# Kernel tuning notes

Hardware: AMD Instinct MI355X
Metric: run time of the kernel (lower is better)

Reference implementation:

```python
import jax, jax.numpy as jnp
import numpy as np

PRED_STEPS = 12
N_NEG = 100
TEMP = 0.1
EPS = 1e-12


def _l2norm(x):
    # matches torch F.normalize(dim=-1): x / max(||x||, eps)
    n = jnp.sqrt(jnp.sum(x * x, axis=-1, keepdims=True))
    return x / jnp.maximum(n, EPS)


def setup_inputs() -> dict:
    key = jax.random.key(0)
    k1, k2, k3, k4 = jax.random.split(key, 4)
    B, T, D = 8, 256, 256
    context = jax.random.normal(k1, (B, T, D), dtype=jnp.float32)
    targets = jax.random.normal(k2, (B, T, D), dtype=jnp.float32)
    W = jax.random.normal(k3, (PRED_STEPS, D, D), dtype=jnp.float32) * (1.0 / np.sqrt(D))
    b = jax.random.normal(k4, (PRED_STEPS, D), dtype=jnp.float32) * 0.01
    return {"context": context, "targets": targets, "W": W, "b": b}


def reference(context, targets, W, b):
    B, T, D = context.shape
    neg_key = jax.random.key(1234)
    total = jnp.zeros((), dtype=context.dtype)
    count = 0
    for step in range(1, PRED_STEPS + 1):
        if T - step <= 0:
            break
        T2 = T - step
        ctx = context[:, :T2, :]                        # (B,T2,D)
        pos = targets[:, step:, :]                      # (B,T2,D)
        # per-step linear predictor (torch Linear: x @ W^T + b)
        query = jnp.einsum('btd,ed->bte', ctx, W[step - 1]) + b[step - 1]
        query = _l2norm(query)
        pos_n = _l2norm(pos)                            # also serves as the negative pool
        pos_sim = jnp.sum(query * pos_n, axis=-1, keepdims=True) / TEMP  # (B,T2,1)
        # random in-batch negatives (deterministic per-step key)
        neg_idx = jax.random.randint(jax.random.fold_in(neg_key, step),
                                     (B, T2, N_NEG), 0, B * T2)
        flat = pos_n.reshape(B * T2, D)
        negs = flat[neg_idx]                            # (B,T2,K,D) gather
        neg_sim = jnp.einsum('btd,btkd->btk', query, negs) / TEMP  # (B,T2,K)
        logits = jnp.concatenate([pos_sim, neg_sim], axis=-1)      # (B,T2,1+K)
        # cross-entropy with label 0 == -log_softmax(logits)[..., 0], averaged
        loss_step = -jnp.mean(jax.nn.log_softmax(logits, axis=-1)[..., 0])
        total = total + loss_step
        count += 1
    return total / max(count, 1)
```

## Files before the change

### kernel.cpp

```cpp
#include <hip/hip_runtime.h>
#include <stdint.h>

#define BB 8
#define TT 256
#define DD 256
#define NSTEP 12
#define NNEG 100
#define NPART (255 * BB * NSTEP)

typedef _Float16 h2 __attribute__((ext_vector_type(2)));
typedef _Float16 f16x8 __attribute__((ext_vector_type(8)));
typedef float f32x4 __attribute__((ext_vector_type(4)));

#if __has_builtin(__builtin_amdgcn_fdot2)
__device__ __forceinline__ float fdot2(h2 a, h2 b, float c) {
  return __builtin_amdgcn_fdot2(a, b, c, false);
}
#else
__device__ __forceinline__ float fdot2(h2 a, h2 b, float c) {
  return c + (float)a.x * (float)b.x + (float)a.y * (float)b.y;
}
#endif

__device__ __forceinline__ h2 e5m2_lo(uint32_t w) {
#if __has_builtin(__builtin_amdgcn_perm)
  uint32_t r = __builtin_amdgcn_perm(0u, w, 0x010c000cu);
#else
  uint32_t r = ((w & 0xFFu) << 8) | ((w & 0xFF00u) << 16);
#endif
  union { uint32_t u; h2 h; } c; c.u = r; return c.h;
}
__device__ __forceinline__ h2 e5m2_hi(uint32_t w) {
#if __has_builtin(__builtin_amdgcn_perm)
  uint32_t r = __builtin_amdgcn_perm(0u, w, 0x030c020cu);
#else
  uint32_t r = ((w >> 8) & 0xFF00u) | ((w >> 16) & 0xFF000000u) | (((w >> 16) & 0xFFu) << 8);
#endif
  union { uint32_t u; h2 h; } c; c.u = r; return c.h;
}

__device__ __forceinline__ uint32_t f32_to_e5m2(float f) {
  union { _Float16 h; uint16_t u; } c; c.h = (_Float16)f;
  uint16_t h = c.u;
  return (uint32_t)((uint16_t)(h + (uint16_t)0x7F + (uint16_t)((h >> 8) & 1u)) >> 8) & 0xFFu;
}

__host__ __device__ __forceinline__ void tf2x32(uint32_t k0, uint32_t k1,
                                                uint32_t x0, uint32_t x1,
                                                uint32_t &y0, uint32_t &y1) {
  const uint32_t ks2 = k0 ^ k1 ^ 0x1BD11BDAu;
  x0 += k0; x1 += k1;
#define TF_R(r) { x0 += x1; x1 = (x1 << (r)) | (x1 >> (32 - (r))); x1 ^= x0; }
  TF_R(13) TF_R(15) TF_R(26) TF_R(6)
  x0 += k1; x1 += ks2 + 1u;
  TF_R(17) TF_R(29) TF_R(16) TF_R(24)
  x0 += ks2; x1 += k0 + 2u;
  TF_R(13) TF_R(15) TF_R(26) TF_R(6)
  x0 += k0; x1 += k1 + 3u;
  TF_R(17) TF_R(29) TF_R(16) TF_R(24)
  x0 += k1; x1 += ks2 + 4u;
  TF_R(13) TF_R(15) TF_R(26) TF_R(6)
  x0 += ks2; x1 += k0 + 5u;
#undef TF_R
  y0 = x0; y1 = x1;
}

struct IdxParams {
  uint32_t k1x[NSTEP], k1y[NSTEP], k2x[NSTEP], k2y[NSTEP];
  uint32_t mult[NSTEP];
  uint32_t Msp[NSTEP], Ssp[NSTEP], Asp[NSTEP];
  uint32_t Mt2[NSTEP], St2[NSTEP], At2[NSTEP];
};

static void magicu(uint32_t d, uint32_t* M, uint32_t* s, uint32_t* a) {
  uint32_t p, nc, delta, q1, r1, q2, r2;
  *a = 0;
  nc = 0xFFFFFFFFu - (0u - d) % d;
  p = 31;
  q1 = 0x80000000u / nc; r1 = 0x80000000u - q1 * nc;
  q2 = 0x7FFFFFFFu / d;  r2 = 0x7FFFFFFFu - q2 * d;
  do {
    p = p + 1;
    if (r1 >= nc - r1) { q1 = 2*q1 + 1; r1 = 2*r1 - nc; }
    else               { q1 = 2*q1;     r1 = 2*r1; }
    if (r2 + 1 >= d - r2) {
      if (q2 >= 0x7FFFFFFFu) *a = 1;
      q2 = 2*q2 + 1; r2 = 2*r2 + 1 - d;
    } else {
      if (q2 >= 0x80000000u) *a = 1;
      q2 = 2*q2; r2 = 2*r2 + 1;
    }
    delta = d - 1 - r2;
  } while (p < 64 && (q1 < delta || (q1 == delta && r1 == 0)));
  *M = q2 + 1; *s = p - 32;
}

__device__ __forceinline__ uint32_t mdiv(uint32_t n, uint32_t M, uint32_t s, uint32_t a) {
  uint32_t q = __umulhi(n, M);
  if (a) { q = ((n - q) >> 1) + q; return q >> (s - 1); }
  return q >> s;
}

__global__ __launch_bounds__(256) void prep_kernel(const float* __restrict__ tgt,
                                                   const float* __restrict__ ctx,
                                                   const float* __restrict__ W,
                                                   uint8_t* __restrict__ tn8,
                                                   _Float16* __restrict__ ctxh,
                                                   _Float16* __restrict__ Wh) {
  const int bx = blockIdx.x;
  const int tid = threadIdx.x;
  const int lane = tid & 63;
  if (bx < 512) {
    const int row = bx * 4 + (tid >> 6);
    float4 v = ((const float4*)(tgt + (size_t)row * DD))[lane];
    float ss = v.x*v.x + v.y*v.y + v.z*v.z + v.w*v.w;
#pragma unroll
    for (int off = 1; off < 64; off <<= 1) ss += __shfl_xor(ss, off, 64);
    const float sc = 1.0f / fmaxf(sqrtf(ss), 1e-12f);
    const uint32_t p = f32_to_e5m2(v.x * sc) | (f32_to_e5m2(v.y * sc) << 8)
                     | (f32_to_e5m2(v.z * sc) << 16) | (f32_to_e5m2(v.w * sc) << 24);
    ((uint32_t*)(tn8 + (size_t)row * DD))[lane] = p;
  } else {
    union { _Float16 h[4]; uint2 u; } o;
    if (bx < 1024) {
      const int row = (bx - 512) * 4 + (tid >> 6);
      float4 v = ((const float4*)(ctx + (size_t)row * DD))[lane];
      o.h[0] = (_Float16)v.x; o.h[1] = (_Float16)v.y;
      o.h[2] = (_Float16)v.z; o.h[3] = (_Float16)v.w;
      ((uint2*)(ctxh + (size_t)row * DD))[lane] = o.u;
    } else {
      const int row = (bx - 1024) * 4 + (tid >> 6);
      float4 v = ((const float4*)(W + (size_t)row * DD))[lane];
      o.h[0] = (_Float16)v.x; o.h[1] = (_Float16)v.y;
      o.h[2] = (_Float16)v.z; o.h[3] = (_Float16)v.w;
      ((uint2*)(Wh + (size_t)row * DD))[lane] = o.u;
    }
  }
}

__global__ __launch_bounds__(256) void qgemm_mfma_kernel(const _Float16* __restrict__ ctxh,
                                                         const _Float16* __restrict__ Wh,
                                                         const float* __restrict__ bias,
                                                         _Float16* __restrict__ qnh) {
  const int mt  = blockIdx.x;
  const int s   = blockIdx.y;
  const int tid = threadIdx.x;
  const int w   = tid >> 6;
  const int lane = tid & 63;
  const int sl = lane & 15;
  const int q  = lane >> 4;
  const int m0 = mt * 32;

  const _Float16* Arow0 = ctxh + ((size_t)(m0 + sl)) * DD + q * 8;
  const _Float16* Arow1 = Arow0 + (size_t)16 * DD;
  const _Float16* Bbase = Wh + (size_t)s * DD * DD + ((size_t)(w * 64 + sl)) * DD + q * 8;

  f32x4 acc[2][4];
#pragma unroll
  for (int mi = 0; mi < 2; ++mi)
#pragma unroll
    for (int nt = 0; nt < 4; ++nt) acc[mi][nt] = f32x4{0, 0, 0, 0};

#pragma unroll
  for (int k0 = 0; k0 < 8; ++k0) {
    const f16x8 a0 = *(const f16x8*)(Arow0 + k0 * 32);
    const f16x8 a1 = *(const f16x8*)(Arow1 + k0 * 32);
#pragma unroll
    for (int nt = 0; nt < 4; ++nt) {
      const f16x8 b = *(const f16x8*)(Bbase + (size_t)nt * 16 * DD + k0 * 32);
      acc[0][nt] = __builtin_amdgcn_mfma_f32_16x16x32_f16(a0, b, acc[0][nt], 0, 0, 0);
      acc[1][nt] = __builtin_amdgcn_mfma_f32_16x16x32_f16(a1, b, acc[1][nt], 0, 0, 0);
    }
  }
  const float* bp = bias + (size_t)s * DD + w * 64 + sl;
  __shared__ float part[4][32];
#pragma unroll
  for (int mi = 0; mi < 2; ++mi) {
#pragma unroll
    for (int nt = 0; nt < 4; ++nt) {
      const float bv = bp[nt * 16];
#pragma unroll
      for (int r = 0; r < 4; ++r) acc[mi][nt][r] += bv;
    }
    float ss[4];
#pragma unroll
    for (int r = 0; r < 4; ++r) {
      float v = 0.f;
#pragma unroll
      for (int nt = 0; nt < 4; ++nt) v += acc[mi][nt][r] * acc[mi][nt][r];
      ss[r] = v;
    }
#pragma unroll
    for (int off = 1; off < 16; off <<= 1) {
#pragma unroll
      for (int r = 0; r < 4; ++r) ss[r] += __shfl_xor(ss[r], off, 64);
    }
    if (sl == 0) {
#pragma unroll
      for (int r = 0; r < 4; ++r) part[w][mi * 16 + q * 4 + r] = ss[r];
    }
  }
  __syncthreads();
#pragma unroll
  for (int mi = 0; mi < 2; ++mi) {
#pragma unroll
    for (int r = 0; r < 4; ++r) {
      const int row = q * 4 + r;
      const float tot = part[0][mi * 16 + row] + part[1][mi * 16 + row]
                      + part[2][mi * 16 + row] + part[3][mi * 16 + row];
      const float sc = 1.0f / fmaxf(sqrtf(tot), 1e-12f);
      _Float16* outp = qnh + (((size_t)s * (BB * TT)) + m0 + mi * 16 + row) * DD + w * 64 + sl;
#pragma unroll
      for (int nt = 0; nt < 4; ++nt) outp[nt * 16] = (_Float16)(acc[mi][nt][r] * sc);
    }
  }
}

__global__ __launch_bounds__(128) void score_kernel(const IdxParams P,
                                                    const _Float16* __restrict__ qnh,
                                                    const uint8_t* __restrict__ tn8,
                                                    float* __restrict__ partial) {
  const int t    = blockIdx.x;
  const int b    = blockIdx.y;
  const int si   = blockIdx.z;
  const int step = si + 1;
  const int T2   = TT - step;
  const int lin  = (si * BB + b) * 255 + t;
  const int tid  = threadIdx.x;
  if (t >= T2) { if (tid == 0) partial[lin] = 0.f; return; }

  __shared__ int   rowIdx[NNEG + 1];
  __shared__ float logit[NNEG + 1];

  if (tid < NNEG) {
    const uint32_t span = (uint32_t)(BB * T2);
    const uint32_t j = (uint32_t)((b * T2 + t) * NNEG + tid);
    uint32_t h0, h1, l0, l1;
    tf2x32(P.k1x[si], P.k1y[si], 0u, j, h0, h1);
    tf2x32(P.k2x[si], P.k2y[si], 0u, j, l0, l1);
    const uint32_t Msp = P.Msp[si], Ssp = P.Ssp[si], Asp = P.Asp[si];
    const uint32_t hm = h0 - mdiv(h0, Msp, Ssp, Asp) * span;
    const uint32_t lm = l0 - mdiv(l0, Msp, Ssp, Asp) * span;
    const uint32_t off = hm * P.mult[si] + lm;
    const uint32_t om = off - mdiv(off, Msp, Ssp, Asp) * span;
    const uint32_t bb = mdiv(om, P.Mt2[si], P.St2[si], P.At2[si]);
    const uint32_t tt = om - bb * (uint32_t)T2;
    rowIdx[tid + 1] = (int)(bb * TT + tt + (uint32_t)step);
  } else if (tid == NNEG) {
    rowIdx[0] = b * TT + t + step;
  }

  const int g  = tid >> 2;
  const int gl = tid & 3;
  const _Float16* qrow = qnh + (((size_t)si * (BB * TT)) + b * TT + t) * DD;
  uint4 qv[8];
#pragma unroll
  for (int c = 0; c < 4; ++c) {
    qv[c * 2]     = *(const uint4*)(qrow + c * 64 + gl * 16);
    qv[c * 2 + 1] = *(const uint4*)(qrow + c * 64 + gl * 16 + 8);
  }
  __syncthreads();

#pragma unroll
  for (int r = 0; r < 4; ++r) {
    const int k = r * 32 + g;
    if (k <= NNEG) {
      const uint8_t* prow = tn8 + (size_t)rowIdx[k] * DD;
      float d0 = 0.f, d1 = 0.f, d2 = 0.f, d3 = 0.f;
#pragma unroll
      for (int c = 0; c < 4; ++c) {
        const uint4 pv = *(const uint4*)(prow + c * 64 + gl * 16);
        union { uint4 u; h2 h[4]; } qa, qb;
        qa.u = qv[c * 2]; qb.u = qv[c * 2 + 1];
        d0 = fdot2(qa.h[0], e5m2_lo(pv.x), d0);
        d1 = fdot2(qa.h[1], e5m2_hi(pv.x), d1);
        d2 = fdot2(qa.h[2], e5m2_lo(pv.y), d2);
        d3 = fdot2(qa.h[3], e5m2_hi(pv.y), d3);
        d0 = fdot2(qb.h[0], e5m2_lo(pv.z), d0);
        d1 = fdot2(qb.h[1], e5m2_hi(pv.z), d1);
        d2 = fdot2(qb.h[2], e5m2_lo(pv.w), d2);
        d3 = fdot2(qb.h[3], e5m2_hi(pv.w), d3);
      }
      float d = (d0 + d1) + (d2 + d3);
      d += __shfl_xor(d, 1, 64);
      d += __shfl_xor(d, 2, 64);
      if (gl == 0) logit[k] = d * 10.0f;
    }
  }
  __syncthreads();

  if (tid < 64) {
    const int lane = tid;
    const float a = logit[lane];
    const float c = (lane + 64 <= NNEG) ? logit[lane + 64] : -1e30f;
    float m = fmaxf(a, c);
#pragma unroll
    for (int off = 1; off < 64; off <<= 1) m = fmaxf(m, __shfl_xor(m, off, 64));
    float e = __expf(a - m) + ((lane + 64 <= NNEG) ? __expf(c - m) : 0.f);
#pragma unroll
    for (int off = 1; off < 64; off <<= 1) e += __shfl_xor(e, off, 64);
    if (lane == 0) {
      const float lse = m + logf(e);
      partial[lin] = (lse - logit[0]) / (12.0f * (float)(BB * T2));
    }
  }
}

__global__ __launch_bounds__(1024) void final_sum_kernel(const float* __restrict__ partial,
                                                         float* __restrict__ out) {
  __shared__ float wsum[16];
  const int tid = threadIdx.x;
  float s = 0.f;
  const float4* p4 = (const float4*)partial;
  for (int i = tid; i < NPART / 4; i += 1024) {
    const float4 v = p4[i];
    s += v.x + v.y + v.z + v.w;
  }
#pragma unroll
  for (int off = 1; off < 64; off <<= 1) s += __shfl_xor(s, off, 64);
  if ((tid & 63) == 0) wsum[tid >> 6] = s;
  __syncthreads();
  if (tid == 0) {
    float tot = 0.f;
#pragma unroll
    for (int i = 0; i < 16; ++i) tot += wsum[i];
    out[0] = tot;
  }
}

extern "C" void kernel_launch(void* const* d_in, const int* in_sizes, int n_in,
                              void* d_out, int out_size, void* d_ws, size_t ws_size,
                              hipStream_t stream) {
  const float* ctx  = (const float*)d_in[0];
  const float* tgt  = (const float*)d_in[1];
  const float* W    = (const float*)d_in[2];
  const float* bias = (const float*)d_in[3];
  float* out = (float*)d_out;

  uint8_t* tn8   = (uint8_t*)d_ws;
  _Float16* ctxh = (_Float16*)(tn8 + (size_t)BB * TT * DD);
  _Float16* Wh   = ctxh + (size_t)BB * TT * DD;
  _Float16* qnh  = Wh + (size_t)NSTEP * DD * DD;
  float* partial = (float*)(qnh + (size_t)NSTEP * BB * TT * DD);

  IdxParams P;
  for (int s = 0; s < NSTEP; ++s) {
    uint32_t a, b;
    tf2x32(0u, 1234u, 0u, (uint32_t)(s + 1), a, b);
    uint32_t h1a, h1b, h2a, h2b;
    tf2x32(a, b, 0u, 2u, h1a, h1b);
    tf2x32(a, b, 1u, 3u, h2a, h2b);
    P.k1x[s] = h1a; P.k1y[s] = h1b; P.k2x[s] = h2a; P.k2y[s] = h2b;
    const uint32_t T2 = (uint32_t)(TT - (s + 1));
    const uint32_t span = 8u * T2;
    uint32_t m = 65536u % span;
    P.mult[s] = (uint32_t)(((uint64_t)m * m) % span);
    magicu(span, &P.Msp[s], &P.Ssp[s], &P.Asp[s]);
    magicu(T2,   &P.Mt2[s], &P.St2[s], &P.At2[s]);
  }

  hipLaunchKernelGGL(prep_kernel, dim3(1792), dim3(256), 0, stream,
                     tgt, ctx, W, tn8, ctxh, Wh);
  hipLaunchKernelGGL(qgemm_mfma_kernel, dim3(64, NSTEP), dim3(256), 0, stream,
                     ctxh, Wh, bias, qnh);
  hipLaunchKernelGGL(score_kernel, dim3(255, BB, NSTEP), dim3(128), 0, stream,
                     P, qnh, tn8, partial);
  hipLaunchKernelGGL(final_sum_kernel, dim3(1), dim3(1024), 0, stream, partial, out);
}
```

Measured before the change: 133.2 us.

## Score negatives with fp8 MFMA over 16-query tiles and precomputed index table

```diff
diff --git a/kernel.cpp b/kernel.cpp
--- a/kernel.cpp
+++ b/kernel.cpp
@@ -6,43 +6,42 @@
 #define DD 256
 #define NSTEP 12
 #define NNEG 100
-#define NPART (255 * BB * NSTEP)
-
-typedef _Float16 h2 __attribute__((ext_vector_type(2)));
+#define SLOTP 104
+
 typedef _Float16 f16x8 __attribute__((ext_vector_type(8)));
 typedef float f32x4 __attribute__((ext_vector_type(4)));
 
-#if __has_builtin(__builtin_amdgcn_fdot2)
-__device__ __forceinline__ float fdot2(h2 a, h2 b, float c) {
-  return __builtin_amdgcn_fdot2(a, b, c, false);
-}
+__device__ __forceinline__ uint32_t f32_to_e4m3(float x) {
+#if __has_builtin(__builtin_amdgcn_cvt_pk_fp8_f32)
+  return (uint32_t)__builtin_amdgcn_cvt_pk_fp8_f32(x, x, 0, false) & 0xFFu;
 #else
-__device__ __forceinline__ float fdot2(h2 a, h2 b, float c) {
-  return c + (float)a.x * (float)b.x + (float)a.y * (float)b.y;
-}
+  union { float f; uint32_t u; } c; c.f = x;
+  uint32_t s = (c.u >> 24) & 0x80u;
+  float a = fabsf(x);
+  if (!(a < 448.f)) return s | 0x7Eu;
+  int e; float mf = frexpf(a, &e); (void)mf;
+  e -= 1;
+  int E = e < -6 ? -6 : e;
+  float q = nearbyintf(ldexpf(a, 3 - E));
+  int qi = (int)q;
+  if (qi == 0) return s;
+  while (qi >= 16) { qi >>= 1; ++E; }
+  if (qi < 8) return s | (uint32_t)qi;
+  return s | ((uint32_t)(E + 7) << 3) | (uint32_t)(qi & 7);
 #endif
-
-__device__ __forceinline__ h2 e5m2_lo(uint32_t w) {
-#if __has_builtin(__builtin_amdgcn_perm)
-  uint32_t r = __builtin_amdgcn_perm(0u, w, 0x010c000cu);
+}
+
+__device__ __forceinline__ uint32_t f32x4_to_e4m3x4(float x, float y, float z, float w) {
+#if __has_builtin(__builtin_amdgcn_cvt_pk_fp8_f32)
+  int lo = __builtin_amdgcn_cvt_pk_fp8_f32(x, y, 0, false);
+  return (uint32_t)__builtin_amdgcn_cvt_pk_fp8_f32(z, w, lo, true);
 #else
-  uint32_t r = ((w & 0xFFu) << 8) | ((w & 0xFF00u) << 16);
+  return f32_to_e4m3(x) | (f32_to_e4m3(y) << 8) | (f32_to_e4m3(z) << 16) | (f32_to_e4m3(w) << 24);
 #endif
-  union { uint32_t u; h2 h; } c; c.u = r; return c.h;
-}
-__device__ __forceinline__ h2 e5m2_hi(uint32_t w) {
-#if __has_builtin(__builtin_amdgcn_perm)
-  uint32_t r = __builtin_amdgcn_perm(0u, w, 0x030c020cu);
-#else
-  uint32_t r = ((w >> 8) & 0xFF00u) | ((w >> 16) & 0xFF000000u) | (((w >> 16) & 0xFFu) << 8);
-#endif
-  union { uint32_t u; h2 h; } c; c.u = r; return c.h;
-}
-
-__device__ __forceinline__ uint32_t f32_to_e5m2(float f) {
-  union { _Float16 h; uint16_t u; } c; c.h = (_Float16)f;
-  uint16_t h = c.u;
-  return (uint32_t)((uint16_t)(h + (uint16_t)0x7F + (uint16_t)((h >> 8) & 1u)) >> 8) & 0xFFu;
+}
+
+__device__ __forceinline__ long pk64(uint2 v) {
+  union { uint2 u; long l; } c; c.u = v; return c.l;
 }
 
 __host__ __device__ __forceinline__ void tf2x32(uint32_t k0, uint32_t k1,
@@ -101,26 +100,30 @@
   return q >> s;
 }
 
-__global__ __launch_bounds__(256) void prep_kernel(const float* __restrict__ tgt,
+__global__ __launch_bounds__(256) void prep_kernel(const IdxParams P,
+                                                   const float* __restrict__ tgt,
                                                    const float* __restrict__ ctx,
                                                    const float* __restrict__ W,
                                                    uint8_t* __restrict__ tn8,
                                                    _Float16* __restrict__ ctxh,
-                                                   _Float16* __restrict__ Wh) {
+                                                   _Float16* __restrict__ Wh,
+                                                   uint16_t* __restrict__ idxTab,
+                                                   float* __restrict__ out) {
   const int bx = blockIdx.x;
   const int tid = threadIdx.x;
-  const int lane = tid & 63;
+  if (bx == 0 && tid == 0) out[0] = 0.f;
   if (bx < 512) {
+    const int lane = tid & 63;
     const int row = bx * 4 + (tid >> 6);
     float4 v = ((const float4*)(tgt + (size_t)row * DD))[lane];
     float ss = v.x*v.x + v.y*v.y + v.z*v.z + v.w*v.w;
 #pragma unroll
     for (int off = 1; off < 64; off <<= 1) ss += __shfl_xor(ss, off, 64);
     const float sc = 1.0f / fmaxf(sqrtf(ss), 1e-12f);
-    const uint32_t p = f32_to_e5m2(v.x * sc) | (f32_to_e5m2(v.y * sc) << 8)
-                     | (f32_to_e5m2(v.z * sc) << 16) | (f32_to_e5m2(v.w * sc) << 24);
-    ((uint32_t*)(tn8 + (size_t)row * DD))[lane] = p;
-  } else {
+    ((uint32_t*)(tn8 + (size_t)row * DD))[lane] =
+        f32x4_to_e4m3x4(v.x * sc, v.y * sc, v.z * sc, v.w * sc);
+  } else if (bx < 1792) {
+    const int lane = tid & 63;
     union { _Float16 h[4]; uint2 u; } o;
     if (bx < 1024) {
       const int row = (bx - 512) * 4 + (tid >> 6);
@@ -135,13 +138,44 @@
       o.h[2] = (_Float16)v.z; o.h[3] = (_Float16)v.w;
       ((uint2*)(Wh + (size_t)row * DD))[lane] = o.u;
     }
+  } else {
+    const int ib = bx - 1792;
+    const int si = ib / 832;
+    const int step = si + 1;
+    const uint32_t T2 = (uint32_t)(TT - step);
+    const uint32_t nloc = (uint32_t)(ib - si * 832) * 256u + (uint32_t)tid;
+    const uint32_t m = nloc / 104u;
+    const uint32_t slot = nloc - m * 104u;
+    const uint32_t t = m & 255u;
+    const uint32_t b = m >> 8;
+    uint32_t v = 0u;
+    if (t < T2 && slot <= (uint32_t)NNEG) {
+      if (slot == 0u) {
+        v = b * TT + t + (uint32_t)step;
+      } else {
+        const uint32_t j = (b * T2 + t) * NNEG + (slot - 1u);
+        uint32_t h0, h1, l0, l1;
+        tf2x32(P.k1x[si], P.k1y[si], 0u, j, h0, h1);
+        tf2x32(P.k2x[si], P.k2y[si], 0u, j, l0, l1);
+        const uint32_t span = 8u * T2;
+        const uint32_t Msp = P.Msp[si], Ssp = P.Ssp[si], Asp = P.Asp[si];
+        const uint32_t hm = h0 - mdiv(h0, Msp, Ssp, Asp) * span;
+        const uint32_t lm = l0 - mdiv(l0, Msp, Ssp, Asp) * span;
+        const uint32_t off = hm * P.mult[si] + lm;
+        const uint32_t om = off - mdiv(off, Msp, Ssp, Asp) * span;
+        const uint32_t bbq = mdiv(om, P.Mt2[si], P.St2[si], P.At2[si]);
+        const uint32_t tt = om - bbq * T2;
+        v = bbq * TT + tt + (uint32_t)step;
+      }
+    }
+    idxTab[(size_t)si * (2048u * 104u) + nloc] = (uint16_t)v;
   }
 }
 
 __global__ __launch_bounds__(256) void qgemm_mfma_kernel(const _Float16* __restrict__ ctxh,
                                                          const _Float16* __restrict__ Wh,
                                                          const float* __restrict__ bias,
-                                                         _Float16* __restrict__ qnh) {
+                                                         uint8_t* __restrict__ qn8) {
   const int mt  = blockIdx.x;
   const int s   = blockIdx.y;
   const int tid = threadIdx.x;
@@ -209,123 +243,96 @@
       const float tot = part[0][mi * 16 + row] + part[1][mi * 16 + row]
                       + part[2][mi * 16 + row] + part[3][mi * 16 + row];
       const float sc = 1.0f / fmaxf(sqrtf(tot), 1e-12f);
-      _Float16* outp = qnh + (((size_t)s * (BB * TT)) + m0 + mi * 16 + row) * DD + w * 64 + sl;
-#pragma unroll
-      for (int nt = 0; nt < 4; ++nt) outp[nt * 16] = (_Float16)(acc[mi][nt][r] * sc);
-    }
-  }
-}
-
-__global__ __launch_bounds__(128) void score_kernel(const IdxParams P,
-                                                    const _Float16* __restrict__ qnh,
+      uint8_t* outp = qn8 + (((size_t)s * (BB * TT)) + m0 + mi * 16 + row) * DD + w * 64 + sl;
+#pragma unroll
+      for (int nt = 0; nt < 4; ++nt)
+        outp[nt * 16] = (uint8_t)f32_to_e4m3(acc[mi][nt][r] * sc);
+    }
+  }
+}
+
+__global__ __launch_bounds__(256) void score_kernel(const uint8_t* __restrict__ qn8,
                                                     const uint8_t* __restrict__ tn8,
-                                                    float* __restrict__ partial) {
-  const int t    = blockIdx.x;
-  const int b    = blockIdx.y;
-  const int si   = blockIdx.z;
+                                                    const uint16_t* __restrict__ idxTab,
+                                                    float* __restrict__ out) {
+  const int tc = blockIdx.x;
+  const int b  = blockIdx.y;
+  const int si = blockIdx.z;
   const int step = si + 1;
-  const int T2   = TT - step;
-  const int lin  = (si * BB + b) * 255 + t;
-  const int tid  = threadIdx.x;
-  if (t >= T2) { if (tid == 0) partial[lin] = 0.f; return; }
-
-  __shared__ int   rowIdx[NNEG + 1];
-  __shared__ float logit[NNEG + 1];
-
-  if (tid < NNEG) {
-    const uint32_t span = (uint32_t)(BB * T2);
-    const uint32_t j = (uint32_t)((b * T2 + t) * NNEG + tid);
-    uint32_t h0, h1, l0, l1;
-    tf2x32(P.k1x[si], P.k1y[si], 0u, j, h0, h1);
-    tf2x32(P.k2x[si], P.k2y[si], 0u, j, l0, l1);
-    const uint32_t Msp = P.Msp[si], Ssp = P.Ssp[si], Asp = P.Asp[si];
-    const uint32_t hm = h0 - mdiv(h0, Msp, Ssp, Asp) * span;
-    const uint32_t lm = l0 - mdiv(l0, Msp, Ssp, Asp) * span;
-    const uint32_t off = hm * P.mult[si] + lm;
-    const uint32_t om = off - mdiv(off, Msp, Ssp, Asp) * span;
-    const uint32_t bb = mdiv(om, P.Mt2[si], P.St2[si], P.At2[si]);
-    const uint32_t tt = om - bb * (uint32_t)T2;
-    rowIdx[tid + 1] = (int)(bb * TT + tt + (uint32_t)step);
-  } else if (tid == NNEG) {
-    rowIdx[0] = b * TT + t + step;
-  }
-
-  const int g  = tid >> 2;
-  const int gl = tid & 3;
-  const _Float16* qrow = qnh + (((size_t)si * (BB * TT)) + b * TT + t) * DD;
-  uint4 qv[8];
-#pragma unroll
-  for (int c = 0; c < 4; ++c) {
-    qv[c * 2]     = *(const uint4*)(qrow + c * 64 + gl * 16);
-    qv[c * 2 + 1] = *(const uint4*)(qrow + c * 64 + gl * 16 + 8);
-  }
+  const int T2 = TT - step;
+  const int t0 = tc * 16;
+  const int tid = threadIdx.x;
+  const int w   = tid >> 6;
+  const int l   = tid & 63;
+  const int q16 = l & 15;
+  const int kh  = l >> 4;
+
+  __shared__ int   ridx[16][SLOTP];
+  __shared__ float logit[16][105];
+  __shared__ float bsum;
+  if (tid == 0) bsum = 0.f;
+
+  const uint16_t* g16 = idxTab + (size_t)(((si * BB + b) * TT) + t0) * SLOTP;
+  if (tid < 208) {
+    const int r = tid / 13, c = tid % 13;
+    uint4 v = *(const uint4*)(g16 + (size_t)r * SLOTP + c * 8);
+    int* dst = &ridx[r][c * 8];
+    dst[0] = (int)(v.x & 0xFFFFu); dst[1] = (int)(v.x >> 16);
+    dst[2] = (int)(v.y & 0xFFFFu); dst[3] = (int)(v.y >> 16);
+    dst[4] = (int)(v.z & 0xFFFFu); dst[5] = (int)(v.z >> 16);
+    dst[6] = (int)(v.w & 0xFFFFu); dst[7] = (int)(v.w >> 16);
+  }
+
+  const uint8_t* qrow = qn8 + ((size_t)(si * (BB * TT) + b * TT + t0 + q16)) * DD + kh * 8;
+  uint2 qv[8];
+#pragma unroll
+  for (int kk = 0; kk < 8; ++kk) qv[kk] = *(const uint2*)(qrow + kk * 32);
+
   __syncthreads();
 
-#pragma unroll
-  for (int r = 0; r < 4; ++r) {
-    const int k = r * 32 + g;
-    if (k <= NNEG) {
-      const uint8_t* prow = tn8 + (size_t)rowIdx[k] * DD;
-      float d0 = 0.f, d1 = 0.f, d2 = 0.f, d3 = 0.f;
-#pragma unroll
-      for (int c = 0; c < 4; ++c) {
-        const uint4 pv = *(const uint4*)(prow + c * 64 + gl * 16);
-        union { uint4 u; h2 h[4]; } qa, qb;
-        qa.u = qv[c * 2]; qb.u = qv[c * 2 + 1];
-        d0 = fdot2(qa.h[0], e5m2_lo(pv.x), d0);
-        d1 = fdot2(qa.h[1], e5m2_hi(pv.x), d1);
-        d2 = fdot2(qa.h[2], e5m2_lo(pv.y), d2);
-        d3 = fdot2(qa.h[3], e5m2_hi(pv.y), d3);
-        d0 = fdot2(qb.h[0], e5m2_lo(pv.z), d0);
-        d1 = fdot2(qb.h[1], e5m2_hi(pv.z), d1);
-        d2 = fdot2(qb.h[2], e5m2_lo(pv.w), d2);
-        d3 = fdot2(qb.h[3], e5m2_hi(pv.w), d3);
+  const bool diag = (kh == (q16 >> 2));
+  const int  rr   = l & 3;
+#pragma unroll 2
+  for (int slot = w; slot <= NNEG; slot += 4) {
+    const int R = ridx[q16][slot];
+    const uint8_t* kr = tn8 + (size_t)R * DD + kh * 8;
+    uint2 av[8];
+#pragma unroll
+    for (int kk = 0; kk < 8; ++kk) av[kk] = *(const uint2*)(kr + kk * 32);
+    f32x4 acc0 = {0, 0, 0, 0}, acc1 = {0, 0, 0, 0};
+#pragma unroll
+    for (int kk = 0; kk < 8; kk += 2) {
+      acc0 = __builtin_amdgcn_mfma_f32_16x16x32_fp8_fp8(pk64(av[kk]),     pk64(qv[kk]),     acc0, 0, 0, 0);
+      acc1 = __builtin_amdgcn_mfma_f32_16x16x32_fp8_fp8(pk64(av[kk + 1]), pk64(qv[kk + 1]), acc1, 0, 0, 0);
+    }
+    const float d0 = rr == 0 ? acc0[0] : rr == 1 ? acc0[1] : rr == 2 ? acc0[2] : acc0[3];
+    const float d1 = rr == 0 ? acc1[0] : rr == 1 ? acc1[1] : rr == 2 ? acc1[2] : acc1[3];
+    if (diag) logit[q16][slot] = (d0 + d1) * 10.0f;
+  }
+  __syncthreads();
+
+  if (tid < 128) {
+    const int q = tid >> 3, i = tid & 7;
+    const int t = t0 + q;
+    if (t < T2) {
+      float m = -1e30f;
+      for (int k = i; k <= NNEG; k += 8) m = fmaxf(m, logit[q][k]);
+      m = fmaxf(m, __shfl_xor(m, 1, 64));
+      m = fmaxf(m, __shfl_xor(m, 2, 64));
+      m = fmaxf(m, __shfl_xor(m, 4, 64));
+      float e = 0.f;
+      for (int k = i; k <= NNEG; k += 8) e += __expf(logit[q][k] - m);
+      e += __shfl_xor(e, 1, 64);
+      e += __shfl_xor(e, 2, 64);
+      e += __shfl_xor(e, 4, 64);
+      if (i == 0) {
+        const float lse = m + logf(e);
+        atomicAdd(&bsum, (lse - logit[q][0]) / (12.0f * (float)(BB * T2)));
       }
-      float d = (d0 + d1) + (d2 + d3);
-      d += __shfl_xor(d, 1, 64);
-      d += __shfl_xor(d, 2, 64);
-      if (gl == 0) logit[k] = d * 10.0f;
     }
   }
   __syncthreads();
-
-  if (tid < 64) {
-    const int lane = tid;
-    const float a = logit[lane];
-    const float c = (lane + 64 <= NNEG) ? logit[lane + 64] : -1e30f;
-    float m = fmaxf(a, c);
-#pragma unroll
-    for (int off = 1; off < 64; off <<= 1) m = fmaxf(m, __shfl_xor(m, off, 64));
-    float e = __expf(a - m) + ((lane + 64 <= NNEG) ? __expf(c - m) : 0.f);
-#pragma unroll
-    for (int off = 1; off < 64; off <<= 1) e += __shfl_xor(e, off, 64);
-    if (lane == 0) {
-      const float lse = m + logf(e);
-      partial[lin] = (lse - logit[0]) / (12.0f * (float)(BB * T2));
-    }
-  }
-}
-
-__global__ __launch_bounds__(1024) void final_sum_kernel(const float* __restrict__ partial,
-                                                         float* __restrict__ out) {
-  __shared__ float wsum[16];
-  const int tid = threadIdx.x;
-  float s = 0.f;
-  const float4* p4 = (const float4*)partial;
-  for (int i = tid; i < NPART / 4; i += 1024) {
-    const float4 v = p4[i];
-    s += v.x + v.y + v.z + v.w;
-  }
-#pragma unroll
-  for (int off = 1; off < 64; off <<= 1) s += __shfl_xor(s, off, 64);
-  if ((tid & 63) == 0) wsum[tid >> 6] = s;
-  __syncthreads();
-  if (tid == 0) {
-    float tot = 0.f;
-#pragma unroll
-    for (int i = 0; i < 16; ++i) tot += wsum[i];
-    out[0] = tot;
-  }
+  if (tid == 0) atomicAdd(out, bsum);
 }
 
 extern "C" void kernel_launch(void* const* d_in, const int* in_sizes, int n_in,
@@ -340,8 +347,8 @@
   uint8_t* tn8   = (uint8_t*)d_ws;
   _Float16* ctxh = (_Float16*)(tn8 + (size_t)BB * TT * DD);
   _Float16* Wh   = ctxh + (size_t)BB * TT * DD;
-  _Float16* qnh  = Wh + (size_t)NSTEP * DD * DD;
-  float* partial = (float*)(qnh + (size_t)NSTEP * BB * TT * DD);
+  uint8_t* qn8   = (uint8_t*)(Wh + (size_t)NSTEP * DD * DD);
+  uint16_t* idxTab = (uint16_t*)(qn8 + (size_t)NSTEP * BB * TT * DD);
 
   IdxParams P;
   for (int s = 0; s < NSTEP; ++s) {
@@ -359,11 +366,10 @@
     magicu(T2,   &P.Mt2[s], &P.St2[s], &P.At2[s]);
   }
 
-  hipLaunchKernelGGL(prep_kernel, dim3(1792), dim3(256), 0, stream,
-                     tgt, ctx, W, tn8, ctxh, Wh);
+  hipLaunchKernelGGL(prep_kernel, dim3(1792 + 12 * 832), dim3(256), 0, stream,
+                     P, tgt, ctx, W, tn8, ctxh, Wh, idxTab, out);
   hipLaunchKernelGGL(qgemm_mfma_kernel, dim3(64, NSTEP), dim3(256), 0, stream,
-                     ctxh, Wh, bias, qnh);
-  hipLaunchKernelGGL(score_kernel, dim3(255, BB, NSTEP), dim3(128), 0, stream,
-                     P, qnh, tn8, partial);
-  hipLaunchKernelGGL(final_sum_kernel, dim3(1), dim3(1024), 0, stream, partial, out);
-}
+                     ctxh, Wh, bias, qn8);
+  hipLaunchKernelGGL(score_kernel, dim3(16, BB, NSTEP), dim3(256), 0, stream,
+                     qn8, tn8, idxTab, out);
+}
```

New measurement: 237.8 us. 78.5% more time.

## Quantize query and targets to int8 and precompute negative indices in prep

Applied to the files above, without the earlier changes.

```diff
diff --git a/kernel.cpp b/kernel.cpp
--- a/kernel.cpp
+++ b/kernel.cpp
@@ -6,43 +6,27 @@
 #define DD 256
 #define NSTEP 12
 #define NNEG 100
+#define SLOTP 104
 #define NPART (255 * BB * NSTEP)
 
-typedef _Float16 h2 __attribute__((ext_vector_type(2)));
 typedef _Float16 f16x8 __attribute__((ext_vector_type(8)));
 typedef float f32x4 __attribute__((ext_vector_type(4)));
 
-#if __has_builtin(__builtin_amdgcn_fdot2)
-__device__ __forceinline__ float fdot2(h2 a, h2 b, float c) {
-  return __builtin_amdgcn_fdot2(a, b, c, false);
-}
+__device__ __forceinline__ int sdot4(int a, int b, int c) {
+#if __has_builtin(__builtin_amdgcn_sdot4)
+  return __builtin_amdgcn_sdot4(a, b, c, false);
 #else
-__device__ __forceinline__ float fdot2(h2 a, h2 b, float c) {
-  return c + (float)a.x * (float)b.x + (float)a.y * (float)b.y;
-}
+  int s = c;
+#pragma unroll
+  for (int i = 0; i < 4; ++i)
+    s += (int)(int8_t)(a >> (8 * i)) * (int)(int8_t)(b >> (8 * i));
+  return s;
 #endif
-
-__device__ __forceinline__ h2 e5m2_lo(uint32_t w) {
-#if __has_builtin(__builtin_amdgcn_perm)
-  uint32_t r = __builtin_amdgcn_perm(0u, w, 0x010c000cu);
-#else
-  uint32_t r = ((w & 0xFFu) << 8) | ((w & 0xFF00u) << 16);
-#endif
-  union { uint32_t u; h2 h; } c; c.u = r; return c.h;
-}
-__device__ __forceinline__ h2 e5m2_hi(uint32_t w) {
-#if __has_builtin(__builtin_amdgcn_perm)
-  uint32_t r = __builtin_amdgcn_perm(0u, w, 0x030c020cu);
-#else
-  uint32_t r = ((w >> 8) & 0xFF00u) | ((w >> 16) & 0xFF000000u) | (((w >> 16) & 0xFFu) << 8);
-#endif
-  union { uint32_t u; h2 h; } c; c.u = r; return c.h;
-}
-
-__device__ __forceinline__ uint32_t f32_to_e5m2(float f) {
-  union { _Float16 h; uint16_t u; } c; c.h = (_Float16)f;
-  uint16_t h = c.u;
-  return (uint32_t)((uint16_t)(h + (uint16_t)0x7F + (uint16_t)((h >> 8) & 1u)) >> 8) & 0xFFu;
+}
+
+__device__ __forceinline__ int f32_to_i8c(float x) {
+  int v = __float2int_rn(x);
+  return v > 127 ? 127 : (v < -127 ? -127 : v);
 }
 
 __host__ __device__ __forceinline__ void tf2x32(uint32_t k0, uint32_t k1,
@@ -101,26 +85,31 @@
   return q >> s;
 }
 
-__global__ __launch_bounds__(256) void prep_kernel(const float* __restrict__ tgt,
+__global__ __launch_bounds__(256) void prep_kernel(const IdxParams P,
+                                                   const float* __restrict__ tgt,
                                                    const float* __restrict__ ctx,
                                                    const float* __restrict__ W,
-                                                   uint8_t* __restrict__ tn8,
+                                                   int8_t* __restrict__ ti8,
                                                    _Float16* __restrict__ ctxh,
-                                                   _Float16* __restrict__ Wh) {
+                                                   _Float16* __restrict__ Wh,
+                                                   uint16_t* __restrict__ idxTab) {
   const int bx = blockIdx.x;
   const int tid = threadIdx.x;
-  const int lane = tid & 63;
   if (bx < 512) {
+    const int lane = tid & 63;
     const int row = bx * 4 + (tid >> 6);
     float4 v = ((const float4*)(tgt + (size_t)row * DD))[lane];
     float ss = v.x*v.x + v.y*v.y + v.z*v.z + v.w*v.w;
 #pragma unroll
     for (int off = 1; off < 64; off <<= 1) ss += __shfl_xor(ss, off, 64);
-    const float sc = 1.0f / fmaxf(sqrtf(ss), 1e-12f);
-    const uint32_t p = f32_to_e5m2(v.x * sc) | (f32_to_e5m2(v.y * sc) << 8)
-                     | (f32_to_e5m2(v.z * sc) << 16) | (f32_to_e5m2(v.w * sc) << 24);
-    ((uint32_t*)(tn8 + (size_t)row * DD))[lane] = p;
-  } else {
+    const float sc = 127.0f / fmaxf(sqrtf(ss), 1e-12f);
+    const uint32_t p = ((uint32_t)(f32_to_i8c(v.x * sc) & 255))
+                     | ((uint32_t)(f32_to_i8c(v.y * sc) & 255) << 8)
+                     | ((uint32_t)(f32_to_i8c(v.z * sc) & 255) << 16)
+                     | ((uint32_t)(f32_to_i8c(v.w * sc) & 255) << 24);
+    ((uint32_t*)(ti8 + (size_t)row * DD))[lane] = p;
+  } else if (bx < 1792) {
+    const int lane = tid & 63;
     union { _Float16 h[4]; uint2 u; } o;
     if (bx < 1024) {
       const int row = (bx - 512) * 4 + (tid >> 6);
@@ -135,13 +124,44 @@
       o.h[2] = (_Float16)v.z; o.h[3] = (_Float16)v.w;
       ((uint2*)(Wh + (size_t)row * DD))[lane] = o.u;
     }
+  } else {
+    const int ib = bx - 1792;
+    const int si = ib / 832;
+    const int step = si + 1;
+    const uint32_t T2 = (uint32_t)(TT - step);
+    const uint32_t nloc = (uint32_t)(ib - si * 832) * 256u + (uint32_t)tid;
+    const uint32_t m = nloc / 104u;
+    const uint32_t slot = nloc - m * 104u;
+    const uint32_t t = m & 255u;
+    const uint32_t b = m >> 8;
+    uint32_t v = 0u;
+    if (t < T2 && slot <= (uint32_t)NNEG) {
+      if (slot == 0u) {
+        v = b * TT + t + (uint32_t)step;
+      } else {
+        const uint32_t j = (b * T2 + t) * NNEG + (slot - 1u);
+        uint32_t h0, h1, l0, l1;
+        tf2x32(P.k1x[si], P.k1y[si], 0u, j, h0, h1);
+        tf2x32(P.k2x[si], P.k2y[si], 0u, j, l0, l1);
+        const uint32_t span = 8u * T2;
+        const uint32_t Msp = P.Msp[si], Ssp = P.Ssp[si], Asp = P.Asp[si];
+        const uint32_t hm = h0 - mdiv(h0, Msp, Ssp, Asp) * span;
+        const uint32_t lm = l0 - mdiv(l0, Msp, Ssp, Asp) * span;
+        const uint32_t off = hm * P.mult[si] + lm;
+        const uint32_t om = off - mdiv(off, Msp, Ssp, Asp) * span;
+        const uint32_t bbq = mdiv(om, P.Mt2[si], P.St2[si], P.At2[si]);
+        const uint32_t tt = om - bbq * T2;
+        v = bbq * TT + tt + (uint32_t)step;
+      }
+    }
+    idxTab[(size_t)si * (2048u * 104u) + nloc] = (uint16_t)v;
   }
 }
 
 __global__ __launch_bounds__(256) void qgemm_mfma_kernel(const _Float16* __restrict__ ctxh,
                                                          const _Float16* __restrict__ Wh,
                                                          const float* __restrict__ bias,
-                                                         _Float16* __restrict__ qnh) {
+                                                         int8_t* __restrict__ qi8) {
   const int mt  = blockIdx.x;
   const int s   = blockIdx.y;
   const int tid = threadIdx.x;
@@ -208,17 +228,18 @@
       const int row = q * 4 + r;
       const float tot = part[0][mi * 16 + row] + part[1][mi * 16 + row]
                       + part[2][mi * 16 + row] + part[3][mi * 16 + row];
-      const float sc = 1.0f / fmaxf(sqrtf(tot), 1e-12f);
-      _Float16* outp = qnh + (((size_t)s * (BB * TT)) + m0 + mi * 16 + row) * DD + w * 64 + sl;
-#pragma unroll
-      for (int nt = 0; nt < 4; ++nt) outp[nt * 16] = (_Float16)(acc[mi][nt][r] * sc);
-    }
-  }
-}
-
-__global__ __launch_bounds__(128) void score_kernel(const IdxParams P,
-                                                    const _Float16* __restrict__ qnh,
-                                                    const uint8_t* __restrict__ tn8,
+      const float sc = 127.0f / fmaxf(sqrtf(tot), 1e-12f);
+      int8_t* outp = qi8 + (((size_t)s * (BB * TT)) + m0 + mi * 16 + row) * DD + w * 64 + sl;
+#pragma unroll
+      for (int nt = 0; nt < 4; ++nt)
+        outp[nt * 16] = (int8_t)f32_to_i8c(acc[mi][nt][r] * sc);
+    }
+  }
+}
+
+__global__ __launch_bounds__(128) void score_kernel(const int8_t* __restrict__ qi8,
+                                                    const int8_t* __restrict__ ti8,
+                                                    const uint16_t* __restrict__ idxTab,
                                                     float* __restrict__ partial) {
   const int t    = blockIdx.x;
   const int b    = blockIdx.y;
@@ -232,59 +253,35 @@
   __shared__ int   rowIdx[NNEG + 1];
   __shared__ float logit[NNEG + 1];
 
-  if (tid < NNEG) {
-    const uint32_t span = (uint32_t)(BB * T2);
-    const uint32_t j = (uint32_t)((b * T2 + t) * NNEG + tid);
-    uint32_t h0, h1, l0, l1;
-    tf2x32(P.k1x[si], P.k1y[si], 0u, j, h0, h1);
-    tf2x32(P.k2x[si], P.k2y[si], 0u, j, l0, l1);
-    const uint32_t Msp = P.Msp[si], Ssp = P.Ssp[si], Asp = P.Asp[si];
-    const uint32_t hm = h0 - mdiv(h0, Msp, Ssp, Asp) * span;
-    const uint32_t lm = l0 - mdiv(l0, Msp, Ssp, Asp) * span;
-    const uint32_t off = hm * P.mult[si] + lm;
-    const uint32_t om = off - mdiv(off, Msp, Ssp, Asp) * span;
-    const uint32_t bb = mdiv(om, P.Mt2[si], P.St2[si], P.At2[si]);
-    const uint32_t tt = om - bb * (uint32_t)T2;
-    rowIdx[tid + 1] = (int)(bb * TT + tt + (uint32_t)step);
-  } else if (tid == NNEG) {
-    rowIdx[0] = b * TT + t + step;
-  }
+  if (tid <= NNEG)
+    rowIdx[tid] = (int)idxTab[((size_t)si * 2048 + b * 256 + t) * SLOTP + tid];
 
   const int g  = tid >> 2;
   const int gl = tid & 3;
-  const _Float16* qrow = qnh + (((size_t)si * (BB * TT)) + b * TT + t) * DD;
-  uint4 qv[8];
-#pragma unroll
-  for (int c = 0; c < 4; ++c) {
-    qv[c * 2]     = *(const uint4*)(qrow + c * 64 + gl * 16);
-    qv[c * 2 + 1] = *(const uint4*)(qrow + c * 64 + gl * 16 + 8);
-  }
+  const int8_t* qrow = qi8 + ((size_t)si * 2048 + b * 256 + t) * DD;
+  uint4 qv[4];
+#pragma unroll
+  for (int c = 0; c < 4; ++c)
+    qv[c] = *(const uint4*)(qrow + c * 64 + gl * 16);
   __syncthreads();
 
 #pragma unroll
   for (int r = 0; r < 4; ++r) {
     const int k = r * 32 + g;
     if (k <= NNEG) {
-      const uint8_t* prow = tn8 + (size_t)rowIdx[k] * DD;
-      float d0 = 0.f, d1 = 0.f, d2 = 0.f, d3 = 0.f;
+      const int8_t* prow = ti8 + (size_t)rowIdx[k] * DD;
+      int acc = 0;
 #pragma unroll
       for (int c = 0; c < 4; ++c) {
         const uint4 pv = *(const uint4*)(prow + c * 64 + gl * 16);
-        union { uint4 u; h2 h[4]; } qa, qb;
-        qa.u = qv[c * 2]; qb.u = qv[c * 2 + 1];
-        d0 = fdot2(qa.h[0], e5m2_lo(pv.x), d0);
-        d1 = fdot2(qa.h[1], e5m2_hi(pv.x), d1);
-        d2 = fdot2(qa.h[2], e5m2_lo(pv.y), d2);
-        d3 = fdot2(qa.h[3], e5m2_hi(pv.y), d3);
-        d0 = fdot2(qb.h[0], e5m2_lo(pv.z), d0);
-        d1 = fdot2(qb.h[1], e5m2_hi(pv.z), d1);
-        d2 = fdot2(qb.h[2], e5m2_lo(pv.w), d2);
-        d3 = fdot2(qb.h[3], e5m2_hi(pv.w), d3);
+        acc = sdot4((int)qv[c].x, (int)pv.x, acc);
+        acc = sdot4((int)qv[c].y, (int)pv.y, acc);
+        acc = sdot4((int)qv[c].z, (int)pv.z, acc);
+        acc = sdot4((int)qv[c].w, (int)pv.w, acc);
       }
-      float d = (d0 + d1) + (d2 + d3);
-      d += __shfl_xor(d, 1, 64);
-      d += __shfl_xor(d, 2, 64);
-      if (gl == 0) logit[k] = d * 10.0f;
+      acc += __shfl_xor(acc, 1, 64);
+      acc += __shfl_xor(acc, 2, 64);
+      if (gl == 0) logit[k] = (float)acc * (10.0f / 16129.0f);
     }
   }
   __syncthreads();
@@ -337,11 +334,12 @@
   const float* bias = (const float*)d_in[3];
   float* out = (float*)d_out;
 
-  uint8_t* tn8   = (uint8_t*)d_ws;
-  _Float16* ctxh = (_Float16*)(tn8 + (size_t)BB * TT * DD);
+  int8_t* ti8    = (int8_t*)d_ws;
+  _Float16* ctxh = (_Float16*)(ti8 + (size_t)BB * TT * DD);
   _Float16* Wh   = ctxh + (size_t)BB * TT * DD;
-  _Float16* qnh  = Wh + (size_t)NSTEP * DD * DD;
-  float* partial = (float*)(qnh + (size_t)NSTEP * BB * TT * DD);
+  int8_t* qi8    = (int8_t*)(Wh + (size_t)NSTEP * DD * DD);
+  uint16_t* idxTab = (uint16_t*)(qi8 + (size_t)NSTEP * BB * TT * DD);
+  float* partial = (float*)(idxTab + (size_t)NSTEP * 2048 * SLOTP);
 
   IdxParams P;
   for (int s = 0; s < NSTEP; ++s) {
@@ -359,11 +357,11 @@
     magicu(T2,   &P.Mt2[s], &P.St2[s], &P.At2[s]);
   }
 
-  hipLaunchKernelGGL(prep_kernel, dim3(1792), dim3(256), 0, stream,
-                     tgt, ctx, W, tn8, ctxh, Wh);
+  hipLaunchKernelGGL(prep_kernel, dim3(1792 + 12 * 832), dim3(256), 0, stream,
+                     P, tgt, ctx, W, ti8, ctxh, Wh, idxTab);
   hipLaunchKernelGGL(qgemm_mfma_kernel, dim3(64, NSTEP), dim3(256), 0, stream,
-                     ctxh, Wh, bias, qnh);
+                     ctxh, Wh, bias, qi8);
   hipLaunchKernelGGL(score_kernel, dim3(255, BB, NSTEP), dim3(128), 0, stream,
-                     P, qnh, tn8, partial);
+                     qi8, ti8, idxTab, partial);
   hipLaunchKernelGGL(final_sum_kernel, dim3(1), dim3(1024), 0, stream, partial, out);
 }
```

After: 130.2 us (median of 2 runs). 2.3% less time.
